# Kernel tuning notes

Hardware: AMD Instinct MI355X
Metric: run time of the kernel (lower is better)

Reference implementation:

```python
import jax, jax.numpy as jnp
import numpy as np

DIM, DEPTH, HEADS, DIM_HEAD, MLP = 1024, 4, 16, 64, 4096
INNER = HEADS * DIM_HEAD
B, N = 2, 1024


def _ln(x, g, b, eps=1e-5):
    mu = jnp.mean(x, axis=-1, keepdims=True)
    var = jnp.mean(jnp.square(x - mu), axis=-1, keepdims=True)
    return (x - mu) * jax.lax.rsqrt(var + eps) * g + b


def setup_inputs() -> dict:
    key = jax.random.key(0)
    ks = jax.random.split(key, 8)
    s = 0.02
    return {
        "x": jax.random.normal(ks[0], (B, N, DIM), jnp.float32),
        "mask": jax.random.randint(ks[1], (B, N, N), 0, 2, jnp.int32),
        "ln1_g": jnp.ones((DEPTH, DIM), jnp.float32),
        "ln1_b": jnp.zeros((DEPTH, DIM), jnp.float32),
        "qkv_w": jax.random.normal(ks[2], (DEPTH, DIM, 3 * INNER), jnp.float32) * s,
        "out_w": jax.random.normal(ks[3], (DEPTH, INNER, DIM), jnp.float32) * s,
        "out_b": jnp.zeros((DEPTH, DIM), jnp.float32),
        "ln2_g": jnp.ones((DEPTH, DIM), jnp.float32),
        "ln2_b": jnp.zeros((DEPTH, DIM), jnp.float32),
        "ff1_w": jax.random.normal(ks[4], (DEPTH, DIM, MLP), jnp.float32) * s,
        "ff1_b": jnp.zeros((DEPTH, MLP), jnp.float32),
        "ff2_w": jax.random.normal(ks[5], (DEPTH, MLP, DIM), jnp.float32) * s,
        "ff2_b": jnp.zeros((DEPTH, DIM), jnp.float32),
    }


def reference(x, mask, ln1_g, ln1_b, qkv_w, out_w, out_b, ln2_g, ln2_b,
              ff1_w, ff1_b, ff2_w, ff2_b):
    scale = DIM_HEAD ** -0.5
    masked = (mask == 0)[:, None, :, :]  # [B,1,N,N], True -> fill -1e9
    b, n, _ = x.shape
    for l in range(DEPTH):
        # --- prenorm attention ---
        h = _ln(x, ln1_g[l], ln1_b[l])
        qkv = h @ qkv_w[l]  # [B,N,3*INNER]
        q, k, v = jnp.split(qkv, 3, axis=-1)
        q = q.reshape(b, n, HEADS, DIM_HEAD).transpose(0, 2, 1, 3)
        k = k.reshape(b, n, HEADS, DIM_HEAD).transpose(0, 2, 1, 3)
        v = v.reshape(b, n, HEADS, DIM_HEAD).transpose(0, 2, 1, 3)
        dots = jnp.einsum('bhqd,bhkd->bhqk', q, k) * scale
        dots = jnp.where(masked, jnp.float32(-1e9), dots)
        attn = jax.nn.softmax(dots, axis=-1)
        o = jnp.einsum('bhqk,bhkd->bhqd', attn, v)
        o = o.transpose(0, 2, 1, 3).reshape(b, n, INNER)
        x = o @ out_w[l] + out_b[l] + x
        # --- prenorm feedforward ---
        h = _ln(x, ln2_g[l], ln2_b[l])
        h = jax.nn.gelu(h @ ff1_w[l] + ff1_b[l], approximate=False)
        x = h @ ff2_w[l] + ff2_b[l] + x
    return x
```

## Files before the change

kernel.cpp:

```cpp
#include <hip/hip_runtime.h>
#include <stdint.h>

#define DIMM 1024
#define NSEQ 1024
#define BB 2
#define HEADSN 16
#define MLPD 4096
#define DEPTHN 4
#define MROWS (BB*NSEQ)
#define VSTR 10240

typedef __bf16 bf16x8 __attribute__((ext_vector_type(8)));
typedef float f32x4 __attribute__((ext_vector_type(4)));

__device__ __forceinline__ float bf2f(unsigned short u) {
    union { uint32_t i; float f; } x; x.i = ((uint32_t)u) << 16; return x.f;
}
__device__ __forceinline__ unsigned short f2bf(float f) {
    union { uint32_t i; float f; } x; x.f = f;
    uint32_t r = x.i + 0x7fffu + ((x.i >> 16) & 1u);
    return (unsigned short)(r >> 16);
}
__device__ __forceinline__ float loadf(const void* p, size_t i, int f32) {
    return f32 ? ((const float*)p)[i] : bf2f(((const unsigned short*)p)[i]);
}
__device__ __forceinline__ uint32_t cvt_pk_bf16(float lo, float hi) {
    uint32_t r;
    asm("v_cvt_pk_bf16_f32 %0, %1, %2" : "=v"(r) : "v"(lo), "v"(hi));
    return r;
}

__device__ __forceinline__ void gl_lds16(const unsigned short* g, unsigned short* l) {
    __builtin_amdgcn_global_load_lds(
        (const __attribute__((address_space(1))) uint32_t*)g,
        (__attribute__((address_space(3))) uint32_t*)l,
        16, 0, 0);
}

__device__ __forceinline__ void wait_vm2() { asm volatile("s_waitcnt vmcnt(2)" ::: "memory"); }
__device__ __forceinline__ void wait_vm0() { asm volatile("s_waitcnt vmcnt(0)" ::: "memory"); }
__device__ __forceinline__ void barrier_sync() {
    asm volatile("" ::: "memory");
    __builtin_amdgcn_s_barrier();
    asm volatile("" ::: "memory");
}

__global__ __launch_bounds__(256) void sniff_kernel(const unsigned short* __restrict__ x,
                                                    int* __restrict__ flag) {
    __shared__ int cnt[256];
    int tid = threadIdx.x;
    int c = 0;
    for (int i = tid * 2; i < 65536; i += 512) {
        int e = (x[i] >> 7) & 0xFF;
        if (e >= 0x8A) c++;
    }
    cnt[tid] = c;
    __syncthreads();
    for (int s = 128; s > 0; s >>= 1) {
        if (tid < s) cnt[tid] += cnt[tid + s];
        __syncthreads();
    }
    if (tid == 0) flag[0] = (cnt[0] > 32) ? 1 : 0;
}

__global__ __launch_bounds__(256) void cvt_x(const void* __restrict__ x, float* __restrict__ xf,
                                             const int* __restrict__ flag) {
    int f = flag[0];
    int i = blockIdx.x * 256 + threadIdx.x;
    xf[i] = loadf(x, i, f);
}
__global__ __launch_bounds__(256) void store_out(const float* __restrict__ xf, void* __restrict__ out,
                                                 const int* __restrict__ flag) {
    int f = flag[0];
    int i = blockIdx.x * 256 + threadIdx.x;
    float v = xf[i];
    if (f) ((float*)out)[i] = v;
    else   ((unsigned short*)out)[i] = f2bf(v);
}
__global__ __launch_bounds__(256) void conv_all(const void* s0, const void* s1, const void* s2,
                                                const void* s3, const void* s4, const void* s5,
                                                const void* s6, unsigned short* __restrict__ dst,
                                                const int* __restrict__ flag) {
    int f = flag[0];
    const void* src; int len, off;
    switch (blockIdx.y) {
        case 0: src = s0; len = 1024; off = 0;    break;
        case 1: src = s1; len = 1024; off = 1024; break;
        case 2: src = s2; len = 1024; off = 2048; break;
        case 3: src = s3; len = 1024; off = 3072; break;
        case 4: src = s4; len = 1024; off = 4096; break;
        case 5: src = s5; len = 1024; off = 5120; break;
        default: src = s6; len = 4096; off = 6144; break;
    }
    int i = blockIdx.x * 256 + threadIdx.x;
    if (i < DEPTHN * len) {
        int l = i / len, o = i - l * len;
        dst[l * VSTR + off + o] = f2bf(loadf(src, i, f));
    }
}

__global__ __launch_bounds__(256) void transpose_conv(const void* __restrict__ in, size_t srcOffE,
                                                      unsigned short* __restrict__ out,
                                                      int K, int N, const int* __restrict__ flag) {
    int f = flag[0];
    __shared__ unsigned short t[32][33];
    int n0 = blockIdx.x * 32, k0 = blockIdx.y * 32;
    int tx = threadIdx.x, ty = threadIdx.y;
#pragma unroll
    for (int i = 0; i < 4; i++) {
        int k = k0 + ty + i * 8;
        t[ty + i * 8][tx] = f2bf(loadf(in, srcOffE + (size_t)k * N + n0 + tx, f));
    }
    __syncthreads();
#pragma unroll
    for (int i = 0; i < 4; i++) {
        int n = n0 + ty + i * 8;
        out[(size_t)n * K + k0 + tx] = t[tx][ty + i * 8];
    }
}

__global__ __launch_bounds__(256) void vt_kernel(const unsigned short* __restrict__ qkv,
                                                 unsigned short* __restrict__ vt) {
    __shared__ unsigned short t[32][33];
    int b = blockIdx.z;
    int c0 = blockIdx.x * 32, k0 = blockIdx.y * 32;
    int tx = threadIdx.x, ty = threadIdx.y;
#pragma unroll
    for (int i = 0; i < 4; i++) {
        int k = k0 + ty + i * 8;
        t[ty + i * 8][tx] = qkv[(size_t)(b * 1024 + k) * 3072 + 2048 + c0 + tx];
    }
    __syncthreads();
#pragma unroll
    for (int i = 0; i < 4; i++) {
        int c = c0 + ty + i * 8;
        vt[(size_t)(b * 1024 + c) * 1024 + k0 + tx] = t[tx][ty + i * 8];
    }
}

__global__ __launch_bounds__(256) void mask_pack(const int* __restrict__ mask,
                                                 unsigned long long* __restrict__ bits) {
    int wid = (blockIdx.x * 256 + threadIdx.x) >> 6;
    int lane = threadIdx.x & 63;
#pragma unroll
    for (int i = 0; i < 16; i++) {
        int w = wid * 16 + i;
        int mv = mask[(size_t)w * 64 + lane];
        unsigned long long bl = __ballot(mv != 0);
        if (lane == 0) bits[w] = bl;
    }
}

__global__ __launch_bounds__(256) void ln_kernel(const float* __restrict__ x,
                                                 const unsigned short* __restrict__ g,
                                                 const unsigned short* __restrict__ bta,
                                                 unsigned short* __restrict__ out) {
    int row = blockIdx.x, tid = threadIdx.x;
    const float* xr = x + (size_t)row * DIMM;
    float v[4]; float s = 0.f, s2 = 0.f;
#pragma unroll
    for (int i = 0; i < 4; i++) { v[i] = xr[tid + i * 256]; s += v[i]; s2 += v[i] * v[i]; }
#pragma unroll
    for (int off = 32; off >= 1; off >>= 1) {
        s  += __shfl_down(s, off, 64);
        s2 += __shfl_down(s2, off, 64);
    }
    __shared__ float rs[4], rs2[4];
    int wv = tid >> 6;
    if ((tid & 63) == 0) { rs[wv] = s; rs2[wv] = s2; }
    __syncthreads();
    s  = rs[0] + rs[1] + rs[2] + rs[3];
    s2 = rs2[0] + rs2[1] + rs2[2] + rs2[3];
    float mu  = s * (1.f / DIMM);
    float var = s2 * (1.f / DIMM) - mu * mu;
    float rr  = rsqrtf(var + 1e-5f);
#pragma unroll
    for (int i = 0; i < 4; i++) {
        int c = tid + i * 256;
        float y = (v[i] - mu) * rr * bf2f(g[c]) + bf2f(bta[c]);
        out[(size_t)row * DIMM + c] = f2bf(y);
    }
}

template <int S, int HAS_LN>
__global__ __launch_bounds__(256) void reduce_ln(const float* __restrict__ slab,
                                                 const unsigned short* __restrict__ bias,
                                                 float* __restrict__ xf,
                                                 const unsigned short* __restrict__ g,
                                                 const unsigned short* __restrict__ bta,
                                                 unsigned short* __restrict__ out) {
    const size_t SL = (size_t)MROWS * DIMM;
    int row = blockIdx.x, tid = threadIdx.x;
    float v[4]; float s = 0.f, s2 = 0.f;
#pragma unroll
    for (int i = 0; i < 4; i++) {
        int c = tid + i * 256;
        size_t idx = (size_t)row * DIMM + c;
        float t = xf[idx] + bf2f(bias[c]);
#pragma unroll
        for (int z = 0; z < S; z++) t += slab[z * SL + idx];
        xf[idx] = t;
        v[i] = t; s += t; s2 += t * t;
    }
    if (HAS_LN) {
#pragma unroll
        for (int off = 32; off >= 1; off >>= 1) {
            s  += __shfl_down(s, off, 64);
            s2 += __shfl_down(s2, off, 64);
        }
        __shared__ float rs[4], rs2[4];
        int wv = tid >> 6;
        if ((tid & 63) == 0) { rs[wv] = s; rs2[wv] = s2; }
        __syncthreads();
        s  = rs[0] + rs[1] + rs[2] + rs[3];
        s2 = rs2[0] + rs2[1] + rs2[2] + rs2[3];
        float mu  = s * (1.f / DIMM);
        float var = s2 * (1.f / DIMM) - mu * mu;
        float rr  = rsqrtf(var + 1e-5f);
#pragma unroll
        for (int i = 0; i < 4; i++) {
            int c = tid + i * 256;
            float y = (v[i] - mu) * rr * bf2f(g[c]) + bf2f(bta[c]);
            out[(size_t)row * DIMM + c] = f2bf(y);
        }
    }
}

template <int MODE, int SPLITK>
__global__ __launch_bounds__(512) void gemm_bt(const unsigned short* __restrict__ A,
                                               const unsigned short* __restrict__ Bt,
                                               const unsigned short* __restrict__ bias,
                                               unsigned short* __restrict__ Cbf,
                                               float* __restrict__ Cres,
                                               int M, int N, int K) {
    __shared__ __align__(16) unsigned short As0[128 * 32];
    __shared__ __align__(16) unsigned short As1[128 * 32];
    __shared__ __align__(16) unsigned short Bs0[128 * 32];
    __shared__ __align__(16) unsigned short Bs1[128 * 32];
    const int tid = threadIdx.x;
    const int mBase = blockIdx.y * 128, nBase = blockIdx.x * 128;
    const int w = tid >> 6, lane = tid & 63;
    const int wm = (w >> 2) * 64, wn = (w & 3) * 32;
    const int quad = lane >> 4, l16 = lane & 15;
    const int kLen = K / SPLITK;
    const int kStart = (SPLITK > 1) ? blockIdx.z * kLen : 0;
    const int NT = kLen / 32;

    f32x4 acc[4][2];
#pragma unroll
    for (int i = 0; i < 4; i++)
#pragma unroll
        for (int j = 0; j < 2; j++) acc[i][j] = (f32x4){0.f, 0.f, 0.f, 0.f};

    const int lr = lane >> 2;
    const int lc = ((lane & 3) ^ ((lr >> 1) & 3)) * 8;
    const int wb = w & 3;
    const unsigned short* G = (w < 4 ? A  + (size_t)(mBase + wb * 32 + lr) * K
                                     : Bt + (size_t)(nBase + wb * 32 + lr) * K)
                              + kStart + lc;
    unsigned short* L0a = (w < 4 ? &As0[(wb * 32) * 32] : &Bs0[(wb * 32) * 32]);
    unsigned short* L1a = L0a + 16 * 32;
    unsigned short* L0b = (w < 4 ? &As1[(wb * 32) * 32] : &Bs1[(wb * 32) * 32]);
    unsigned short* L1b = L0b + 16 * 32;
    const size_t rstep = (size_t)16 * K;

    const int rcb = (quad ^ ((l16 >> 1) & 3)) * 8;

    auto compute_t = [&](const unsigned short* Asb, const unsigned short* Bsb) {
        bf16x8 af[4], bfv[2];
#pragma unroll
        for (int i = 0; i < 4; i++)
            af[i] = *(const bf16x8*)&Asb[(wm + i * 16 + l16) * 32 + rcb];
#pragma unroll
        for (int j = 0; j < 2; j++)
            bfv[j] = *(const bf16x8*)&Bsb[(wn + j * 16 + l16) * 32 + rcb];
#pragma unroll
        for (int i = 0; i < 4; i++)
#pragma unroll
            for (int j = 0; j < 2; j++)
                acc[i][j] = __builtin_amdgcn_mfma_f32_16x16x32_bf16(af[i], bfv[j], acc[i][j], 0, 0, 0);
    };

    gl_lds16(G, L0a);
    gl_lds16(G + rstep, L1a);

    for (int t = 0; t < NT; t += 2) {
        gl_lds16(G + (size_t)(t + 1) * 32,         L0b);
        gl_lds16(G + (size_t)(t + 1) * 32 + rstep, L1b);
        wait_vm2();
        barrier_sync();
        compute_t(As0, Bs0);
        barrier_sync();
        if (t + 2 < NT) {
            gl_lds16(G + (size_t)(t + 2) * 32,         L0a);
            gl_lds16(G + (size_t)(t + 2) * 32 + rstep, L1a);
            wait_vm2();
        } else {
            wait_vm0();
        }
        barrier_sync();
        compute_t(As1, Bs1);
        barrier_sync();
    }

    const size_t slabOff = (MODE == 3) ? (size_t)blockIdx.z * M * N : 0;
#pragma unroll
    for (int i = 0; i < 4; i++) {
#pragma unroll
        for (int j = 0; j < 2; j++) {
#pragma unroll
            for (int r = 0; r < 4; r++) {
                int m = mBase + wm + i * 16 + quad * 4 + r;
                int n = nBase + wn + j * 16 + l16;
                float v = acc[i][j][r];
                size_t idx = (size_t)m * N + n;
                if (MODE == 0) {
                    Cbf[idx] = f2bf(v);
                } else if (MODE == 1) {
                    if (SPLITK > 1) {
                        if (blockIdx.z == 0) v += bf2f(bias[n]);
                        atomicAdd(&Cres[idx], v);
                    } else {
                        Cres[idx] += v + bf2f(bias[n]);
                    }
                } else if (MODE == 2) {
                    float t2 = v + bf2f(bias[n]);
                    float gg = 0.5f * t2 * (1.f + erff(t2 * 0.70710678118f));
                    Cbf[idx] = f2bf(gg);
                } else {
                    Cres[slabOff + idx] = v;
                }
            }
        }
    }
}

__global__ __launch_bounds__(256) void attn_mfma(const unsigned short* __restrict__ qkv,
                                                 const unsigned short* __restrict__ vt,
                                                 const unsigned long long* __restrict__ mbits,
                                                 unsigned short* __restrict__ o) {
    __shared__ __align__(16) unsigned short Ks[64 * 72];
    __shared__ __align__(16) unsigned short Vs[64 * 72];

    const int tid = threadIdx.x, w = tid >> 6, lane = tid & 63;
    const int quad = lane >> 4, l16 = lane & 15;
    const int qt = blockIdx.x, h = blockIdx.y, b = blockIdx.z;

    const size_t qrow = (size_t)(b * NSEQ + qt * 64 + w * 16 + l16) * 3072 + h * 64;
    bf16x8 qf[2];
    qf[0] = *(const bf16x8*)(qkv + qrow + quad * 8);
    qf[1] = *(const bf16x8*)(qkv + qrow + 32 + quad * 8);

    const int srow = tid >> 2, scol = (tid & 3) * 16;
    const unsigned short* kg_base = qkv + (size_t)(b * NSEQ) * 3072 + 1024 + h * 64;
    const unsigned short* vg_base = vt + (size_t)((b * HEADSN + h) * 64 + srow) * 1024;

    f32x4 oacc[4];
#pragma unroll
    for (int j = 0; j < 4; j++) oacc[j] = (f32x4){0.f, 0.f, 0.f, 0.f};
    float m_run = -1e30f, l_run = 0.f;

    const unsigned long long* mb = mbits + ((size_t)(b * NSEQ + qt * 64 + w * 16 + l16)) * 16;

    for (int kt = 0; kt < 16; kt++) {
        __syncthreads();
        {
            const unsigned short* kg = kg_base + (size_t)(kt * 64 + srow) * 3072 + scol;
            uint4 k0 = *(const uint4*)kg;
            uint4 k1 = *(const uint4*)(kg + 8);
            const unsigned short* vg = vg_base + kt * 64 + scol;
            uint4 v0 = *(const uint4*)vg;
            uint4 v1 = *(const uint4*)(vg + 8);
            *(uint4*)&Ks[srow * 72 + scol]     = k0;
            *(uint4*)&Ks[srow * 72 + scol + 8] = k1;
            *(uint4*)&Vs[srow * 72 + scol]     = v0;
            *(uint4*)&Vs[srow * 72 + scol + 8] = v1;
        }
        __syncthreads();

        f32x4 sacc[4];
#pragma unroll
        for (int j = 0; j < 4; j++) sacc[j] = (f32x4){0.f, 0.f, 0.f, 0.f};
#pragma unroll
        for (int ks = 0; ks < 2; ks++) {
#pragma unroll
            for (int j = 0; j < 4; j++) {
                bf16x8 kf = *(const bf16x8*)&Ks[(j * 16 + l16) * 72 + ks * 32 + quad * 8];
                sacc[j] = __builtin_amdgcn_mfma_f32_16x16x32_bf16(kf, qf[ks], sacc[j], 0, 0, 0);
            }
        }

        const unsigned long long mw = mb[kt];

        float t[4][4];
        float mxj[4];
#pragma unroll
        for (int j = 0; j < 4; j++) {
            unsigned nib = (unsigned)(mw >> (quad * 4 + j * 16)) & 0xFu;
#pragma unroll
            for (int r = 0; r < 4; r++) {
                float s = sacc[j][r] * 0.125f;
                t[j][r] = ((nib >> r) & 1u) ? s : -1e30f;
            }
            mxj[j] = fmaxf(fmaxf(t[j][0], t[j][1]), fmaxf(t[j][2], t[j][3]));
        }
        float mx = fmaxf(fmaxf(mxj[0], mxj[1]), fmaxf(mxj[2], mxj[3]));
        mx = fmaxf(mx, __shfl_xor(mx, 16, 64));
        mx = fmaxf(mx, __shfl_xor(mx, 32, 64));

        if (!__all(mx <= m_run)) {
            float m_new = fmaxf(m_run, mx);
            float alpha = __expf(m_run - m_new);
            m_run = m_new;
            l_run *= alpha;
            float al[4];
#pragma unroll
            for (int r = 0; r < 4; r++) al[r] = __shfl(alpha, quad * 4 + r, 64);
#pragma unroll
            for (int j = 0; j < 4; j++)
#pragma unroll
                for (int r = 0; r < 4; r++) oacc[j][r] *= al[r];
        }

        float p[4][4];
        float psj[4];
#pragma unroll
        for (int j = 0; j < 4; j++) {
#pragma unroll
            for (int r = 0; r < 4; r++) p[j][r] = __expf(t[j][r] - m_run);
            psj[j] = (p[j][0] + p[j][1]) + (p[j][2] + p[j][3]);
        }
        float ps = (psj[0] + psj[1]) + (psj[2] + psj[3]);
        ps += __shfl_xor(ps, 16, 64);
        ps += __shfl_xor(ps, 32, 64);
        l_run += ps;

        union { uint32_t u[4]; bf16x8 v; } pa[2];
#pragma unroll
        for (int ks = 0; ks < 2; ks++) {
            pa[ks].u[0] = cvt_pk_bf16(p[2 * ks][0],     p[2 * ks][1]);
            pa[ks].u[1] = cvt_pk_bf16(p[2 * ks][2],     p[2 * ks][3]);
            pa[ks].u[2] = cvt_pk_bf16(p[2 * ks + 1][0], p[2 * ks + 1][1]);
            pa[ks].u[3] = cvt_pk_bf16(p[2 * ks + 1][2], p[2 * ks + 1][3]);
        }

#pragma unroll
        for (int ks = 0; ks < 2; ks++) {
#pragma unroll
            for (int j = 0; j < 4; j++) {
                union { ushort4 u[2]; bf16x8 v; } vf;
                const unsigned short* vp = &Vs[(j * 16 + l16) * 72 + ks * 32 + quad * 4];
                vf.u[0] = *(const ushort4*)vp;
                vf.u[1] = *(const ushort4*)(vp + 16);
                oacc[j] = __builtin_amdgcn_mfma_f32_16x16x32_bf16(pa[ks].v, vf.v, oacc[j], 0, 0, 0);
            }
        }
    }

    float inv[4];
#pragma unroll
    for (int r = 0; r < 4; r++) {
        float lr = __shfl(l_run, quad * 4 + r, 64);
        inv[r] = 1.f / lr;
    }
#pragma unroll
    for (int j = 0; j < 4; j++) {
#pragma unroll
        for (int r = 0; r < 4; r++) {
            size_t row = (size_t)(b * NSEQ + qt * 64 + w * 16 + quad * 4 + r);
            o[row * 1024 + h * 64 + j * 16 + l16] = f2bf(oacc[j][r] * inv[r]);
        }
    }
}

extern "C" void kernel_launch(void* const* d_in, const int* in_sizes, int n_in,
                              void* d_out, int out_size, void* d_ws, size_t ws_size,
                              hipStream_t stream) {
    const void* x     = d_in[0];
    const int*  mask  = (const int*)d_in[1];
    const void* ln1_g = d_in[2];
    const void* ln1_b = d_in[3];
    const void* qkv_w = d_in[4];
    const void* out_w = d_in[5];
    const void* out_b = d_in[6];
    const void* ln2_g = d_in[7];
    const void* ln2_b = d_in[8];
    const void* ff1_w = d_in[9];
    const void* ff1_b = d_in[10];
    const void* ff2_w = d_in[11];
    const void* ff2_b = d_in[12];

    char* ws = (char*)d_ws;
    float*          xf     = (float*)ws;
    unsigned short* h_bf   = (unsigned short*)(ws + (8u  << 20));
    unsigned short* qkv_bf = (unsigned short*)(ws + (12u << 20));
    unsigned short* ff_bf  = (unsigned short*)(ws + (12u << 20));
    unsigned short* vt_bf  = (unsigned short*)(ws + (24u << 20));
    unsigned short* o_bf   = (unsigned short*)(ws + (28u << 20));
    unsigned short* wT     = (unsigned short*)(ws + (32u << 20));
    unsigned short* vecs   = (unsigned short*)(ws + (40u << 20));
    int*            flag   = (int*)(ws + (40u << 20) + (128u << 10));
    unsigned long long* mbits = (unsigned long long*)(ws + (40u << 20) + (192u << 10));
    float*          slab   = (float*)(ws + (41u << 20));

    const bool slabs_ok = ws_size >= (74ull << 20);

    sniff_kernel<<<1, 256, 0, stream>>>((const unsigned short*)x, flag);

    conv_all<<<dim3(64, 7), 256, 0, stream>>>(ln1_g, ln1_b, out_b, ln2_g, ln2_b, ff2_b, ff1_b,
                                              vecs, flag);
    mask_pack<<<512, 256, 0, stream>>>(mask, mbits);

    const int nx = MROWS * DIMM;
    cvt_x<<<nx / 256, 256, 0, stream>>>(x, xf, flag);

    for (int l = 0; l < DEPTHN; l++) {
        const unsigned short* lv = vecs + l * VSTR;
        const unsigned short* lvn = vecs + (l + 1) * VSTR;

        if (l == 0)
            ln_kernel<<<MROWS, 256, 0, stream>>>(xf, lv + 0, lv + 1024, h_bf);
        transpose_conv<<<dim3(3072 / 32, 1024 / 32), dim3(32, 8), 0, stream>>>(
            qkv_w, (size_t)l * 1024 * 3072, wT, 1024, 3072, flag);
        gemm_bt<0, 1><<<dim3(3072 / 128, MROWS / 128), 512, 0, stream>>>(
            h_bf, wT, nullptr, qkv_bf, nullptr, MROWS, 3072, 1024);
        vt_kernel<<<dim3(32, 32, BB), dim3(32, 8), 0, stream>>>(qkv_bf, vt_bf);
        attn_mfma<<<dim3(NSEQ / 64, HEADSN, BB), 256, 0, stream>>>(qkv_bf, vt_bf, mbits, o_bf);
        transpose_conv<<<dim3(1024 / 32, 1024 / 32), dim3(32, 8), 0, stream>>>(
            out_w, (size_t)l * 1024 * 1024, wT, 1024, 1024, flag);
        if (slabs_ok) {
            gemm_bt<3, 2><<<dim3(1024 / 128, MROWS / 128, 2), 512, 0, stream>>>(
                o_bf, wT, nullptr, nullptr, slab, MROWS, 1024, 1024);
            reduce_ln<2, 1><<<MROWS, 256, 0, stream>>>(
                slab, lv + 2048, xf, lv + 3072, lv + 4096, h_bf);
        } else {
            gemm_bt<1, 2><<<dim3(1024 / 128, MROWS / 128, 2), 512, 0, stream>>>(
                o_bf, wT, lv + 2048, nullptr, xf, MROWS, 1024, 1024);
            ln_kernel<<<MROWS, 256, 0, stream>>>(xf, lv + 3072, lv + 4096, h_bf);
        }

        transpose_conv<<<dim3(4096 / 32, 1024 / 32), dim3(32, 8), 0, stream>>>(
            ff1_w, (size_t)l * 1024 * 4096, wT, 1024, 4096, flag);
        gemm_bt<2, 1><<<dim3(4096 / 128, MROWS / 128), 512, 0, stream>>>(
            h_bf, wT, lv + 6144, ff_bf, nullptr, MROWS, 4096, 1024);
        transpose_conv<<<dim3(1024 / 32, 4096 / 32), dim3(32, 8), 0, stream>>>(
            ff2_w, (size_t)l * 4096 * 1024, wT, 4096, 1024, flag);
        if (slabs_ok) {
            gemm_bt<3, 4><<<dim3(1024 / 128, MROWS / 128, 4), 512, 0, stream>>>(
                ff_bf, wT, nullptr, nullptr, slab, MROWS, 1024, 4096);
            if (l < DEPTHN - 1)
                reduce_ln<4, 1><<<MROWS, 256, 0, stream>>>(
                    slab, lv + 5120, xf, lvn + 0, lvn + 1024, h_bf);
            else
                reduce_ln<4, 0><<<MROWS, 256, 0, stream>>>(
                    slab, lv + 5120, xf, nullptr, nullptr, nullptr);
        } else {
            gemm_bt<1, 4><<<dim3(1024 / 128, MROWS / 128, 4), 512, 0, stream>>>(
                ff_bf, wT, lv + 5120, nullptr, xf, MROWS, 1024, 4096);
            if (l < DEPTHN - 1)
                ln_kernel<<<MROWS, 256, 0, stream>>>(xf, lvn + 0, lvn + 1024, h_bf);
        }
    }

    store_out<<<nx / 256, 256, 0, stream>>>(xf, d_out, flag);
}
```

Before: 888.2 us.

## Deepen GEMM K-tile to 64, fuse input convert into LN, merge weight transposes

The GEMM K-step per stage doubles from 32 to 64. Each wave now issues four 16-byte global-to-LDS loads per stage, with a new XOR swizzle and two MFMA k-substeps per tile, which halves the number of barriers per K. The separate cvt_x pass is folded into a new ln_raw kernel that converts x to fp32 and computes the first layernorm in one read. The qkv and out weight transposes become a single launch writing to two regions of wT. LDS use per block doubles to 64KB, which may limit occupancy.

```diff
diff --git a/kernel.cpp b/kernel.cpp
--- a/kernel.cpp
+++ b/kernel.cpp
@@ -37,7 +37,7 @@
         16, 0, 0);
 }
 
-__device__ __forceinline__ void wait_vm2() { asm volatile("s_waitcnt vmcnt(2)" ::: "memory"); }
+__device__ __forceinline__ void wait_vm4() { asm volatile("s_waitcnt vmcnt(4)" ::: "memory"); }
 __device__ __forceinline__ void wait_vm0() { asm volatile("s_waitcnt vmcnt(0)" ::: "memory"); }
 __device__ __forceinline__ void barrier_sync() {
     asm volatile("" ::: "memory");
@@ -63,12 +63,6 @@
     if (tid == 0) flag[0] = (cnt[0] > 32) ? 1 : 0;
 }
 
-__global__ __launch_bounds__(256) void cvt_x(const void* __restrict__ x, float* __restrict__ xf,
-                                             const int* __restrict__ flag) {
-    int f = flag[0];
-    int i = blockIdx.x * 256 + threadIdx.x;
-    xf[i] = loadf(x, i, f);
-}
 __global__ __launch_bounds__(256) void store_out(const float* __restrict__ xf, void* __restrict__ out,
                                                  const int* __restrict__ flag) {
     int f = flag[0];
@@ -119,6 +113,36 @@
     }
 }
 
+__global__ __launch_bounds__(256) void transpose_attn(const void* __restrict__ qkvw,
+                                                      const void* __restrict__ outw,
+                                                      int layer, unsigned short* __restrict__ wT,
+                                                      const int* __restrict__ flag) {
+    int f = flag[0];
+    __shared__ unsigned short t[32][33];
+    int id = blockIdx.x;
+    const void* src; int N; size_t soff; unsigned short* dst; int bx, by;
+    if (id < 3072) {
+        N = 3072; bx = id % 96; by = id / 96;
+        src = qkvw; soff = (size_t)layer * 1024 * 3072; dst = wT;
+    } else {
+        id -= 3072; N = 1024; bx = id % 32; by = id / 32;
+        src = outw; soff = (size_t)layer * 1024 * 1024; dst = wT + 3 * 1024 * 1024;
+    }
+    int n0 = bx * 32, k0 = by * 32;
+    int tx = threadIdx.x, ty = threadIdx.y;
+#pragma unroll
+    for (int i = 0; i < 4; i++) {
+        int k = k0 + ty + i * 8;
+        t[ty + i * 8][tx] = f2bf(loadf(src, soff + (size_t)k * N + n0 + tx, f));
+    }
+    __syncthreads();
+#pragma unroll
+    for (int i = 0; i < 4; i++) {
+        int n = n0 + ty + i * 8;
+        dst[(size_t)n * 1024 + k0 + tx] = t[tx][ty + i * 8];
+    }
+}
+
 __global__ __launch_bounds__(256) void vt_kernel(const unsigned short* __restrict__ qkv,
                                                  unsigned short* __restrict__ vt) {
     __shared__ unsigned short t[32][33];
@@ -148,6 +172,44 @@
         int mv = mask[(size_t)w * 64 + lane];
         unsigned long long bl = __ballot(mv != 0);
         if (lane == 0) bits[w] = bl;
+    }
+}
+
+__global__ __launch_bounds__(256) void ln_raw(const void* __restrict__ x, float* __restrict__ xf,
+                                              const unsigned short* __restrict__ g,
+                                              const unsigned short* __restrict__ bta,
+                                              unsigned short* __restrict__ out,
+                                              const int* __restrict__ flag) {
+    int f = flag[0];
+    int row = blockIdx.x, tid = threadIdx.x;
+    size_t base = (size_t)row * DIMM;
+    float v[4]; float s = 0.f, s2 = 0.f;
+#pragma unroll
+    for (int i = 0; i < 4; i++) {
+        int c = tid + i * 256;
+        v[i] = loadf(x, base + c, f);
+        xf[base + c] = v[i];
+        s += v[i]; s2 += v[i] * v[i];
+    }
+#pragma unroll
+    for (int off = 32; off >= 1; off >>= 1) {
+        s  += __shfl_down(s, off, 64);
+        s2 += __shfl_down(s2, off, 64);
+    }
+    __shared__ float rs[4], rs2[4];
+    int wv = tid >> 6;
+    if ((tid & 63) == 0) { rs[wv] = s; rs2[wv] = s2; }
+    __syncthreads();
+    s  = rs[0] + rs[1] + rs[2] + rs[3];
+    s2 = rs2[0] + rs2[1] + rs2[2] + rs2[3];
+    float mu  = s * (1.f / DIMM);
+    float var = s2 * (1.f / DIMM) - mu * mu;
+    float rr  = rsqrtf(var + 1e-5f);
+#pragma unroll
+    for (int i = 0; i < 4; i++) {
+        int c = tid + i * 256;
+        float y = (v[i] - mu) * rr * bf2f(g[c]) + bf2f(bta[c]);
+        out[base + c] = f2bf(y);
     }
 }
 
@@ -233,10 +295,10 @@
                                                unsigned short* __restrict__ Cbf,
                                                float* __restrict__ Cres,
                                                int M, int N, int K) {
-    __shared__ __align__(16) unsigned short As0[128 * 32];
-    __shared__ __align__(16) unsigned short As1[128 * 32];
-    __shared__ __align__(16) unsigned short Bs0[128 * 32];
-    __shared__ __align__(16) unsigned short Bs1[128 * 32];
+    __shared__ __align__(16) unsigned short As0[128 * 64];
+    __shared__ __align__(16) unsigned short Bs0[128 * 64];
+    __shared__ __align__(16) unsigned short As1[128 * 64];
+    __shared__ __align__(16) unsigned short Bs1[128 * 64];
     const int tid = threadIdx.x;
     const int mBase = blockIdx.y * 128, nBase = blockIdx.x * 128;
     const int w = tid >> 6, lane = tid & 63;
@@ -244,7 +306,7 @@
     const int quad = lane >> 4, l16 = lane & 15;
     const int kLen = K / SPLITK;
     const int kStart = (SPLITK > 1) ? blockIdx.z * kLen : 0;
-    const int NT = kLen / 32;
+    const int NT = kLen / 64;
 
     f32x4 acc[4][2];
 #pragma unroll
@@ -252,54 +314,59 @@
 #pragma unroll
         for (int j = 0; j < 2; j++) acc[i][j] = (f32x4){0.f, 0.f, 0.f, 0.f};
 
-    const int lr = lane >> 2;
-    const int lc = ((lane & 3) ^ ((lr >> 1) & 3)) * 8;
     const int wb = w & 3;
-    const unsigned short* G = (w < 4 ? A  + (size_t)(mBase + wb * 32 + lr) * K
-                                     : Bt + (size_t)(nBase + wb * 32 + lr) * K)
-                              + kStart + lc;
-    unsigned short* L0a = (w < 4 ? &As0[(wb * 32) * 32] : &Bs0[(wb * 32) * 32]);
-    unsigned short* L1a = L0a + 16 * 32;
-    unsigned short* L0b = (w < 4 ? &As1[(wb * 32) * 32] : &Bs1[(wb * 32) * 32]);
-    unsigned short* L1b = L0b + 16 * 32;
-    const size_t rstep = (size_t)16 * K;
-
-    const int rcb = (quad ^ ((l16 >> 1) & 3)) * 8;
-
-    auto compute_t = [&](const unsigned short* Asb, const unsigned short* Bsb) {
-        bf16x8 af[4], bfv[2];
+    const int lr8 = lane >> 3;
+    const int sgran = (lane & 7) ^ lr8;
+    const unsigned short* G = (w < 4 ? A  + (size_t)(mBase + wb * 32 + lr8) * K
+                                     : Bt + (size_t)(nBase + wb * 32 + lr8) * K)
+                              + kStart + sgran * 8;
+    unsigned short* S0 = (w < 4 ? As0 : Bs0) + (wb * 32) * 64;
+    unsigned short* S1 = (w < 4 ? As1 : Bs1) + (wb * 32) * 64;
+    const size_t r8 = (size_t)8 * K;
+
+    const int rg0 = (quad ^ (l16 & 7)) * 8;
+    const int rg1 = ((4 + quad) ^ (l16 & 7)) * 8;
+
+    auto stage = [&](unsigned short* S, int t) {
+        const unsigned short* g = G + (size_t)t * 64;
 #pragma unroll
         for (int i = 0; i < 4; i++)
-            af[i] = *(const bf16x8*)&Asb[(wm + i * 16 + l16) * 32 + rcb];
-#pragma unroll
-        for (int j = 0; j < 2; j++)
-            bfv[j] = *(const bf16x8*)&Bsb[(wn + j * 16 + l16) * 32 + rcb];
-#pragma unroll
-        for (int i = 0; i < 4; i++)
+            gl_lds16(g + (size_t)i * r8, S + i * 8 * 64);
+    };
+    auto compute = [&](const unsigned short* Asb, const unsigned short* Bsb) {
+#pragma unroll
+        for (int ks = 0; ks < 2; ks++) {
+            const int rg = ks ? rg1 : rg0;
+            bf16x8 af[4], bfv[2];
+#pragma unroll
+            for (int i = 0; i < 4; i++)
+                af[i] = *(const bf16x8*)&Asb[(wm + i * 16 + l16) * 64 + rg];
 #pragma unroll
             for (int j = 0; j < 2; j++)
-                acc[i][j] = __builtin_amdgcn_mfma_f32_16x16x32_bf16(af[i], bfv[j], acc[i][j], 0, 0, 0);
+                bfv[j] = *(const bf16x8*)&Bsb[(wn + j * 16 + l16) * 64 + rg];
+#pragma unroll
+            for (int i = 0; i < 4; i++)
+#pragma unroll
+                for (int j = 0; j < 2; j++)
+                    acc[i][j] = __builtin_amdgcn_mfma_f32_16x16x32_bf16(af[i], bfv[j], acc[i][j], 0, 0, 0);
+        }
     };
 
-    gl_lds16(G, L0a);
-    gl_lds16(G + rstep, L1a);
-
+    stage(S0, 0);
     for (int t = 0; t < NT; t += 2) {
-        gl_lds16(G + (size_t)(t + 1) * 32,         L0b);
-        gl_lds16(G + (size_t)(t + 1) * 32 + rstep, L1b);
-        wait_vm2();
+        stage(S1, t + 1);
+        wait_vm4();
         barrier_sync();
-        compute_t(As0, Bs0);
+        compute(As0, Bs0);
         barrier_sync();
         if (t + 2 < NT) {
-            gl_lds16(G + (size_t)(t + 2) * 32,         L0a);
-            gl_lds16(G + (size_t)(t + 2) * 32 + rstep, L1a);
-            wait_vm2();
+            stage(S0, t + 2);
+            wait_vm4();
         } else {
             wait_vm0();
         }
         barrier_sync();
-        compute_t(As1, Bs1);
+        compute(As1, Bs1);
         barrier_sync();
     }
 
@@ -511,31 +578,27 @@
                                               vecs, flag);
     mask_pack<<<512, 256, 0, stream>>>(mask, mbits);
 
+    ln_raw<<<MROWS, 256, 0, stream>>>(x, xf, vecs + 0, vecs + 1024, h_bf, flag);
+
     const int nx = MROWS * DIMM;
-    cvt_x<<<nx / 256, 256, 0, stream>>>(x, xf, flag);
 
     for (int l = 0; l < DEPTHN; l++) {
         const unsigned short* lv = vecs + l * VSTR;
         const unsigned short* lvn = vecs + (l + 1) * VSTR;
 
-        if (l == 0)
-            ln_kernel<<<MROWS, 256, 0, stream>>>(xf, lv + 0, lv + 1024, h_bf);
-        transpose_conv<<<dim3(3072 / 32, 1024 / 32), dim3(32, 8), 0, stream>>>(
-            qkv_w, (size_t)l * 1024 * 3072, wT, 1024, 3072, flag);
+        transpose_attn<<<4096, dim3(32, 8), 0, stream>>>(qkv_w, out_w, l, wT, flag);
         gemm_bt<0, 1><<<dim3(3072 / 128, MROWS / 128), 512, 0, stream>>>(
             h_bf, wT, nullptr, qkv_bf, nullptr, MROWS, 3072, 1024);
         vt_kernel<<<dim3(32, 32, BB), dim3(32, 8), 0, stream>>>(qkv_bf, vt_bf);
         attn_mfma<<<dim3(NSEQ / 64, HEADSN, BB), 256, 0, stream>>>(qkv_bf, vt_bf, mbits, o_bf);
-        transpose_conv<<<dim3(1024 / 32, 1024 / 32), dim3(32, 8), 0, stream>>>(
-            out_w, (size_t)l * 1024 * 1024, wT, 1024, 1024, flag);
         if (slabs_ok) {
             gemm_bt<3, 2><<<dim3(1024 / 128, MROWS / 128, 2), 512, 0, stream>>>(
-                o_bf, wT, nullptr, nullptr, slab, MROWS, 1024, 1024);
+                o_bf, wT + 3 * 1024 * 1024, nullptr, nullptr, slab, MROWS, 1024, 1024);
             reduce_ln<2, 1><<<MROWS, 256, 0, stream>>>(
                 slab, lv + 2048, xf, lv + 3072, lv + 4096, h_bf);
         } else {
             gemm_bt<1, 2><<<dim3(1024 / 128, MROWS / 128, 2), 512, 0, stream>>>(
-                o_bf, wT, lv + 2048, nullptr, xf, MROWS, 1024, 1024);
+                o_bf, wT + 3 * 1024 * 1024, lv + 2048, nullptr, xf, MROWS, 1024, 1024);
             ln_kernel<<<MROWS, 256, 0, stream>>>(xf, lv + 3072, lv + 4096, h_bf);
         }
 
```

Result: faster. 843.4 us (-5.0%).
